# Optimization experiments

Measured on AMD Instinct MI355X. Metric: run time of the kernel, lower is better.

## Reference

```python
import jax, jax.numpy as jnp
import numpy as np

B, TXT_T, MEL_T, N_MEL = 8, 200, 800, 80
PAD_MAG = 1.0e12


def setup_inputs() -> dict:
    key = jax.random.key(0)
    k1, k2, k3, k4 = jax.random.split(key, 4)
    mu_logvar = jax.random.normal(k1, (B, TXT_T, 2 * N_MEL), dtype=jnp.float32)
    melspec = jax.random.normal(k2, (B, N_MEL, MEL_T), dtype=jnp.float32)
    # lengths are 1-based (indexed as length-1), keep them in [T//2, T]
    text_lengths = jax.random.randint(k3, (B,), TXT_T // 2, TXT_T + 1)
    mel_lengths = jax.random.randint(k4, (B,), MEL_T // 2, MEL_T + 1)
    return {
        "mu_logvar": mu_logvar,
        "melspec": melspec,
        "text_lengths": text_lengths,
        "mel_lengths": mel_lengths,
    }


def _log_prob_matrix(mu_logvar, melspec):
    # melspec: [B, n_mel, mel_T] -> x: [B, 1, mel_T, n_mel]
    x = jnp.transpose(melspec, (0, 2, 1))[:, None, :, :]
    mu = mu_logvar[:, :, :N_MEL][:, :, None, :]       # [B, txt_T, 1, n_mel]
    logvar = mu_logvar[:, :, N_MEL:][:, :, None, :]   # [B, txt_T, 1, n_mel]
    # -0.5 * mean_over_mel( (x-mu)^2 / exp(logvar) + logvar )
    sq = (x - mu) ** 2
    return (-0.5 * (sq * jnp.exp(-logvar) + logvar)).mean(axis=3)  # [B, txt_T, mel_T]


def reference(mu_logvar, melspec, text_lengths, mel_lengths):
    lp = _log_prob_matrix(mu_logvar, melspec)  # [B, txt_T, mel_T]

    # log_alpha column carry, with a leading pad row (index 0 stays -PAD_MAG)
    init = jnp.full((B, TXT_T + 1), -PAD_MAG, dtype=lp.dtype)
    init = init.at[:, 1].set(lp[:, 0, 0])

    def step(a, lp_t):  # a: [B, txt_T+1], lp_t: [B, txt_T]
        # logsumexp over {stay, advance}; original adds 1e-7 to prev values
        new_rows = jnp.logaddexp(a[:, 1:] + 1e-7, a[:, :-1] + 1e-7) + lp_t
        a = a.at[:, 1:].set(new_rows)
        return a, new_rows

    lp_rest = jnp.moveaxis(lp[:, :, 1:], 2, 0)  # [mel_T-1, B, txt_T]
    _, cols = jax.lax.scan(step, init, lp_rest)  # cols: [mel_T-1, B, txt_T]

    log_alpha = jnp.concatenate(
        [init[:, 1:, None], jnp.moveaxis(cols, 0, 2)], axis=2
    )  # [B, txt_T, mel_T]

    b = jnp.arange(B)
    alpha_last = log_alpha[b, text_lengths - 1, mel_lengths - 1]
    alpha_last = alpha_last / mel_lengths.astype(alpha_last.dtype)
    mdn_loss = -alpha_last.mean()
    return mdn_loss, lp
```

## Files before the change

kernel.cpp:

```cpp
#include <hip/hip_runtime.h>
#include <math.h>

#define BB 8
#define TXT_T 200
#define MEL_T 800
#define N_MEL 80
#define GSTR 256
#define CH 16
#define LOG2E 1.44269504088896340736f
#define LN2   0.69314718055994530942f
#define EPS2  (1e-7f * LOG2E)
#define NPAD  -1.0e12f

#define SBAR()       asm volatile("s_barrier" ::: "memory")
#define WAIT_LGKM0() asm volatile("s_waitcnt lgkmcnt(0)" ::: "memory")

__device__ __forceinline__ float exp2_hw(float x) {
#if __has_builtin(__builtin_amdgcn_exp2f)
    return __builtin_amdgcn_exp2f(x);
#else
    return __expf(LN2 * x);
#endif
}

__device__ __forceinline__ float lse2(float A, float B) {
    float m = fmaxf(A, B);
    float e = exp2_hw(-fabsf(A - B));
    return m + __log2f(1.0f + e);
}

__device__ __forceinline__ float lse3(float A, float B, float C) {
    float m = fmaxf(fmaxf(A, B), C);
    float e = exp2_hw(A - m) + exp2_hw(B - m) + exp2_hw(C - m);
    return m + __log2f(e);
}

__global__ void __launch_bounds__(256) lp_kernel(
        const float* __restrict__ mu_logvar,
        const float* __restrict__ melspec,
        float* __restrict__ out_lp,
        float* __restrict__ lpT) {
    const int bt = blockIdx.x;
    const int b  = bt / TXT_T;
    const int t  = bt % TXT_T;
    const int tid = threadIdx.x;

    __shared__ float s_mu[N_MEL];
    __shared__ float s_ev[N_MEL];
    __shared__ float s_lv[N_MEL];
    __shared__ float s_sumlv;

    if (tid < N_MEL) {
        float mu = mu_logvar[(size_t)bt * (2 * N_MEL) + tid];
        float lv = mu_logvar[(size_t)bt * (2 * N_MEL) + N_MEL + tid];
        s_mu[tid] = mu;
        s_ev[tid] = __expf(-lv);
        s_lv[tid] = lv;
    }
    __syncthreads();
    if (tid == 0) {
        float s = 0.f;
        #pragma unroll
        for (int n = 0; n < N_MEL; ++n) s += s_lv[n];
        s_sumlv = s;
    }
    __syncthreads();

    if (tid < MEL_T / 4) {
        const float4* ms4 = (const float4*)(melspec + (size_t)b * N_MEL * MEL_T);
        float ax = 0.f, ay = 0.f, az = 0.f, aw = 0.f;
        #pragma unroll 8
        for (int n = 0; n < N_MEL; ++n) {
            float4 x = ms4[(size_t)n * (MEL_T / 4) + tid];
            float mu = s_mu[n];
            float ev = s_ev[n];
            float d0 = x.x - mu; ax += d0 * d0 * ev;
            float d1 = x.y - mu; ay += d1 * d1 * ev;
            float d2 = x.z - mu; az += d2 * d2 * ev;
            float d3 = x.w - mu; aw += d3 * d3 * ev;
        }
        const float c = -0.5f / (float)N_MEL;
        float slv = s_sumlv;
        float l0 = c * (ax + slv);
        float l1 = c * (ay + slv);
        float l2 = c * (az + slv);
        float l3 = c * (aw + slv);

        size_t ob = (size_t)bt * MEL_T + tid * 4;
        out_lp[ob + 0] = l0;
        out_lp[ob + 1] = l1;
        out_lp[ob + 2] = l2;
        out_lp[ob + 3] = l3;

        int m0 = tid * 4;
        size_t tb = ((size_t)(b * MEL_T + m0)) * GSTR + t;
        lpT[tb + 0 * GSTR] = l0 * LOG2E + EPS2;
        lpT[tb + 1 * GSTR] = l1 * LOG2E + EPS2;
        lpT[tb + 2 * GSTR] = l2 * LOG2E + EPS2;
        lpT[tb + 3 * GSTR] = l3 * LOG2E + EPS2;
    }
}

__device__ __forceinline__ void stage16(const float* g, float* s, int w, int lane) {
    #pragma unroll
    for (int k = 0; k < 4; ++k) {
        int row = w * 4 + k;
        __builtin_amdgcn_global_load_lds(
            (const __attribute__((address_space(1))) void*)(g + row * GSTR + lane * 4),
            (__attribute__((address_space(3))) void*)(s + row * GSTR),
            16, 0, 0);
    }
}

#define PAIRL(SB, TLOC, TT) do {                                              \
    float* rb_ = &rbuf[par][0];                                               \
    float p_  = (SB)[(TLOC) * GSTR + j];                                      \
    float pm_ = (SB)[(TLOC) * GSTR + jm1];                                    \
    float q_  = (SB)[((TLOC) + 1) * GSTR + j];                                \
    rb_[tid] = r;                                                             \
    WAIT_LGKM0(); SBAR();                                                     \
    float rm1_ = rb_[tm1];                                                    \
    float rm2_ = rb_[tm2];                                                    \
    if (tid == 0) { rm1_ = NPAD; pm_ = NPAD; }                                \
    if (tid <= 1) { rm2_ = NPAD; }                                            \
    if ((TT) == myMel) {          \
        alpha_out[b] = (lse2(r, rm1_) + p_) * scale;                          \
    }                                                                         \
    float s_ = lse2(p_, pm_);                                                 \
    float x_ = r + p_;                                                        \
    float y_ = rm1_ + s_;                                                     \
    float z_ = rm2_ + pm_;                                                    \
    r = lse3(x_, y_, z_) + q_;                                                \
    if ((TT) + 1 == myMel) {          \
        alpha_out[b] = r * scale;                                             \
    }                                                                         \
    par ^= 1;                                                                 \
} while (0)

__global__ void __launch_bounds__(256) scan_kernel(
        const float* __restrict__ lpT,
        const int* __restrict__ text_lengths,
        const int* __restrict__ mel_lengths,
        float* __restrict__ alpha_out) {
    __shared__ float sbuf[2][CH][GSTR];
    __shared__ float rbuf[2][256];
    const int b = blockIdx.x;
    const int tid = threadIdx.x;
    const int w = tid >> 6;
    const int lane = tid & 63;
    const int j   = tid < TXT_T ? tid : (TXT_T - 1);
    const int jm1 = j > 0 ? j - 1 : 0;
    const int tm1 = tid > 0 ? tid - 1 : 0;
    const int tm2 = tid > 1 ? tid - 2 : 0;

    const int melL1 = mel_lengths[b] - 1;
    const int txtL1 = text_lengths[b] - 1;
    const float scale = LN2 / (float)(melL1 + 1);
    const int myMel = (tid == txtL1) ? melL1 : -1;

    const float* gbase = lpT + (size_t)b * MEL_T * GSTR;
    const int clast = melL1 >> 4;

    stage16(gbase,             &sbuf[0][0][0], w, lane);
    stage16(gbase + CH * GSTR, &sbuf[1][0][0], w, lane);

    float r = NPAD;
    int par = 0;

    for (int c = 0; c <= clast; ++c) {
        if (c < clast) { asm volatile("s_waitcnt vmcnt(4)" ::: "memory"); }
        else           { asm volatile("s_waitcnt vmcnt(0)" ::: "memory"); }
        SBAR();

        const float* sb = &sbuf[c & 1][0][0];
        if (c == 0) {
            float lp00 = sb[0];
            r = (tid == 0) ? (lp00 - EPS2) : NPAD;
            {
                float* rb_ = &rbuf[par][0];
                float p_ = sb[GSTR + j];
                rb_[tid] = r;
                WAIT_LGKM0(); SBAR();
                float rm1_ = rb_[tm1];
                if (tid == 0) rm1_ = NPAD;
                r = lse2(r, rm1_) + p_;
                par ^= 1;
            }
            #pragma unroll
            for (int m = 1; m < 8; ++m) {
                PAIRL(sb, 2 * m, 2 * m);
            }
        } else {
            const int tbase = CH * c;
            #pragma unroll
            for (int m = 0; m < 8; ++m) {
                PAIRL(sb, 2 * m, tbase + 2 * m);
            }
        }

        WAIT_LGKM0(); SBAR();
        if (c + 2 <= clast) {
            stage16(gbase + (size_t)(c + 2) * CH * GSTR,
                    &sbuf[c & 1][0][0], w, lane);
        }
    }
}

__global__ void finish_kernel(const float* __restrict__ alpha,
                              float* __restrict__ out) {
    float s = 0.f;
    #pragma unroll
    for (int b = 0; b < BB; ++b) s += alpha[b];
    out[0] = -(s / (float)BB);
}

extern "C" void kernel_launch(void* const* d_in, const int* in_sizes, int n_in,
                              void* d_out, int out_size, void* d_ws, size_t ws_size,
                              hipStream_t stream) {
    const float* mu_logvar    = (const float*)d_in[0];
    const float* melspec      = (const float*)d_in[1];
    const int*   text_lengths = (const int*)d_in[2];
    const int*   mel_lengths  = (const int*)d_in[3];
    float* out = (float*)d_out;

    float* alpha = (float*)d_ws;
    float* lpT   = (float*)d_ws + 64;

    lp_kernel<<<BB * TXT_T, 256, 0, stream>>>(mu_logvar, melspec, out + 1, lpT);
    scan_kernel<<<BB, 256, 0, stream>>>(lpT, text_lengths, mel_lengths, alpha);
    finish_kernel<<<1, 1, 0, stream>>>(alpha, out);
}
```

Before: 126.5 us.

## Wavefront-skewed scan with shuffles and direct global reads instead of LDS staging

The scan kernel now skews each wavefront by one step (wave w processes step i-w), so a barrier only needs to pass the two boundary values between neighbouring waves through a small LDS array. Neighbour values inside a wave come from __shfl_up instead of a full 256-entry LDS round trip, and lp rows are loaded straight from global memory into registers two steps ahead instead of being staged through LDS in chunks. The lpT buffer gets extra padded rows per batch so these lookahead reads stay in bounds. This removes the full-block LDS exchange on the serial critical path. In exchange each step waits on global load latency, and the control flow for the skew is more intricate.

New measurement: 210.3 us. 1.66x slower.

```diff
diff --git a/kernel.cpp b/kernel.cpp
--- a/kernel.cpp
+++ b/kernel.cpp
@@ -6,14 +6,11 @@
 #define MEL_T 800
 #define N_MEL 80
 #define GSTR 256
-#define CH 16
+#define MELPAD 804
 #define LOG2E 1.44269504088896340736f
 #define LN2   0.69314718055994530942f
 #define EPS2  (1e-7f * LOG2E)
 #define NPAD  -1.0e12f
-
-#define SBAR()       asm volatile("s_barrier" ::: "memory")
-#define WAIT_LGKM0() asm volatile("s_waitcnt lgkmcnt(0)" ::: "memory")
 
 __device__ __forceinline__ float exp2_hw(float x) {
 #if __has_builtin(__builtin_amdgcn_exp2f)
@@ -93,7 +90,7 @@
         out_lp[ob + 3] = l3;
 
         int m0 = tid * 4;
-        size_t tb = ((size_t)(b * MEL_T + m0)) * GSTR + t;
+        size_t tb = ((size_t)b * MELPAD + m0) * GSTR + t;
         lpT[tb + 0 * GSTR] = l0 * LOG2E + EPS2;
         lpT[tb + 1 * GSTR] = l1 * LOG2E + EPS2;
         lpT[tb + 2 * GSTR] = l2 * LOG2E + EPS2;
@@ -101,40 +98,35 @@
     }
 }
 
-__device__ __forceinline__ void stage16(const float* g, float* s, int w, int lane) {
-    #pragma unroll
-    for (int k = 0; k < 4; ++k) {
-        int row = w * 4 + k;
-        __builtin_amdgcn_global_load_lds(
-            (const __attribute__((address_space(1))) void*)(g + row * GSTR + lane * 4),
-            (__attribute__((address_space(3))) void*)(s + row * GSTR),
-            16, 0, 0);
-    }
-}
-
-#define PAIRL(SB, TLOC, TT) do {                                              \
-    float* rb_ = &rbuf[par][0];                                               \
-    float p_  = (SB)[(TLOC) * GSTR + j];                                      \
-    float pm_ = (SB)[(TLOC) * GSTR + jm1];                                    \
-    float q_  = (SB)[((TLOC) + 1) * GSTR + j];                                \
-    rb_[tid] = r;                                                             \
-    WAIT_LGKM0(); SBAR();                                                     \
-    float rm1_ = rb_[tm1];                                                    \
-    float rm2_ = rb_[tm2];                                                    \
-    if (tid == 0) { rm1_ = NPAD; pm_ = NPAD; }                                \
-    if (tid <= 1) { rm2_ = NPAD; }                                            \
-    if ((TT) == myMel) {          \
-        alpha_out[b] = (lse2(r, rm1_) + p_) * scale;                          \
+#define BODY(mm, pc, pmc, qc, rmi1, rmi2, rmo1, rmo2, rbiA, rbiB, rboA, rboB) \
+do {                                                                          \
+    const int m_ = (mm);                                                      \
+    if (m_ >= 0 && m_ <= M) {                                                 \
+        float rm1 = rmi1, rm2 = rmi2;                                         \
+        if (lane == 0) { rm1 = w ? rbiA : NPAD; rm2 = w ? rbiB : NPAD; }      \
+        else if (lane == 1) { rm2 = w ? rbiA : NPAD; }                        \
+        float pmv = pmc; if (tid == 0) pmv = NPAD;                            \
+        const int tt = 2 * m_ + 1;                                            \
+        if (tt == myMel) alpha_out[b] = (lse2(r, rm1) + pc) * scale;          \
+        float s_ = lse2(pc, pmv);                                             \
+        float x_ = r + pc, y_ = rm1 + s_, z_ = rm2 + pmv;                     \
+        r = lse3(x_, y_, z_) + qc;                                            \
+        if (tt + 1 == myMel) alpha_out[b] = r * scale;                        \
+        rmo1 = __shfl_up(r, 1);                                               \
+        rmo2 = __shfl_up(r, 2);                                               \
+        if (lane == 62) rbB_s[m_ & 3][w] = r;                                 \
+        if (lane == 63) rbA_s[m_ & 3][w] = r;                                 \
     }                                                                         \
-    float s_ = lse2(p_, pm_);                                                 \
-    float x_ = r + p_;                                                        \
-    float y_ = rm1_ + s_;                                                     \
-    float z_ = rm2_ + pm_;                                                    \
-    r = lse3(x_, y_, z_) + q_;                                                \
-    if ((TT) + 1 == myMel) {          \
-        alpha_out[b] = r * scale;                                             \
+    if (w > 0 && m_ + 1 >= 0 && m_ + 1 <= M) {                                \
+        rboA = rbA_s[m_ & 3][w - 1];                                          \
+        rboB = rbB_s[m_ & 3][w - 1];                                          \
     }                                                                         \
-    par ^= 1;                                                                 \
+    if (m_ + 2 >= 0 && m_ + 2 <= M) {                                         \
+        const float* rp_ = base + (size_t)(2 * m_ + 5) * GSTR;                \
+        pc = rp_[j]; pmc = rp_[jm1]; qc = rp_[GSTR + j];                      \
+    }                                                                         \
+    asm volatile("s_waitcnt lgkmcnt(2)" ::: "memory");                        \
+    __builtin_amdgcn_s_barrier();                                             \
 } while (0)
 
 __global__ void __launch_bounds__(256) scan_kernel(
@@ -142,67 +134,59 @@
         const int* __restrict__ text_lengths,
         const int* __restrict__ mel_lengths,
         float* __restrict__ alpha_out) {
-    __shared__ float sbuf[2][CH][GSTR];
-    __shared__ float rbuf[2][256];
+    __shared__ float rbA_s[4][4];
+    __shared__ float rbB_s[4][4];
     const int b = blockIdx.x;
     const int tid = threadIdx.x;
     const int w = tid >> 6;
     const int lane = tid & 63;
-    const int j   = tid < TXT_T ? tid : (TXT_T - 1);
-    const int jm1 = j > 0 ? j - 1 : 0;
-    const int tm1 = tid > 0 ? tid - 1 : 0;
-    const int tm2 = tid > 1 ? tid - 2 : 0;
+    const int j = tid < TXT_T ? tid : (TXT_T - 1);
+    const int jm1 = j - 1;
 
     const int melL1 = mel_lengths[b] - 1;
     const int txtL1 = text_lengths[b] - 1;
     const float scale = LN2 / (float)(melL1 + 1);
     const int myMel = (tid == txtL1) ? melL1 : -1;
-
-    const float* gbase = lpT + (size_t)b * MEL_T * GSTR;
-    const int clast = melL1 >> 4;
-
-    stage16(gbase,             &sbuf[0][0][0], w, lane);
-    stage16(gbase + CH * GSTR, &sbuf[1][0][0], w, lane);
+    const int M = (melL1 - 1) >> 1;
+
+    const float* base = lpT + (size_t)b * MELPAD * GSTR;
 
     float r = NPAD;
-    int par = 0;
-
-    for (int c = 0; c <= clast; ++c) {
-        if (c < clast) { asm volatile("s_waitcnt vmcnt(4)" ::: "memory"); }
-        else           { asm volatile("s_waitcnt vmcnt(0)" ::: "memory"); }
-        SBAR();
-
-        const float* sb = &sbuf[c & 1][0][0];
-        if (c == 0) {
-            float lp00 = sb[0];
-            r = (tid == 0) ? (lp00 - EPS2) : NPAD;
-            {
-                float* rb_ = &rbuf[par][0];
-                float p_ = sb[GSTR + j];
-                rb_[tid] = r;
-                WAIT_LGKM0(); SBAR();
-                float rm1_ = rb_[tm1];
-                if (tid == 0) rm1_ = NPAD;
-                r = lse2(r, rm1_) + p_;
-                par ^= 1;
-            }
-            #pragma unroll
-            for (int m = 1; m < 8; ++m) {
-                PAIRL(sb, 2 * m, 2 * m);
-            }
+    { float v0 = base[j]; if (tid == 0) r = v0 - EPS2; }
+
+    float rm1E = NPAD, rm2E = NPAD, rm1O = NPAD, rm2O = NPAD;
+    {
+        float t1 = __shfl_up(r, 1);
+        float t2 = __shfl_up(r, 2);
+        if ((w & 1) == 0) { rm1O = t1; rm2O = t2; }
+        else             { rm1E = t1; rm2E = t2; }
+    }
+
+    float pa, pma, qa, pb, pmb, qb;
+    {
+        const float* r1p = base + 1 * GSTR;
+        const float* r3p = base + 3 * GSTR;
+        if ((w & 1) == 0) {
+            pa = r1p[j]; pma = r1p[jm1]; qa = r1p[GSTR + j];
+            pb = r3p[j]; pmb = r3p[jm1]; qb = r3p[GSTR + j];
         } else {
-            const int tbase = CH * c;
-            #pragma unroll
-            for (int m = 0; m < 8; ++m) {
-                PAIRL(sb, 2 * m, tbase + 2 * m);
-            }
+            pb = r1p[j]; pmb = r1p[jm1]; qb = r1p[GSTR + j];
+            pa = r3p[j]; pma = r3p[jm1]; qa = r3p[GSTR + j];
         }
-
-        WAIT_LGKM0(); SBAR();
-        if (c + 2 <= clast) {
-            stage16(gbase + (size_t)(c + 2) * CH * GSTR,
-                    &sbuf[c & 1][0][0], w, lane);
-        }
+    }
+
+    if (lane == 62) rbB_s[3][w] = r;
+    if (lane == 63) rbA_s[3][w] = r;
+    asm volatile("s_waitcnt lgkmcnt(0)" ::: "memory");
+    __builtin_amdgcn_s_barrier();
+
+    float rbEA = NPAD, rbEB = NPAD, rbOA = NPAD, rbOB = NPAD;
+
+    for (int i = 0; i <= M + 3; i += 2) {
+        BODY(i - w,     pa, pma, qa, rm1O, rm2O, rm1E, rm2E,
+             rbOA, rbOB, rbEA, rbEB);
+        BODY(i + 1 - w, pb, pmb, qb, rm1E, rm2E, rm1O, rm2O,
+             rbEA, rbEB, rbOA, rbOB);
     }
 }
 
```
